# Performance work log

Hardware: AMD Instinct MI355X
Metric: run time of the kernel (lower is better)

## Reference

```python
import jax, jax.numpy as jnp
import numpy as np

TEMPERATURE = 0.05
BETA = 1.0
LAMBDA_THRESHOLD = 0.7


def setup_inputs() -> dict:
    key = jax.random.key(0)
    k1, k2 = jax.random.split(key)
    B, D = 8192, 256
    features = jax.random.normal(k1, (B, D), dtype=jnp.float32)
    labels = jax.random.randint(k2, (B,), 0, 100, dtype=jnp.int64)
    return {"features": features, "labels": labels}


def reference(features, labels):
    B = features.shape[0]
    eps = 1e-12
    # L2 normalize rows
    f = features / jnp.maximum(jnp.linalg.norm(features, axis=1, keepdims=True), eps)
    sim = jnp.matmul(f, f.T) / TEMPERATURE                      # [B, B]
    sim_max = jnp.max(sim, axis=1, keepdims=True)               # [B, 1]
    sim_stable = sim - sim_max

    same = (labels[:, None] == labels[None, :])
    eye = jnp.eye(B, dtype=bool)
    pos_mask = same & ~eye                                       # [B, B] bool

    # Denominator: logsumexp over all non-self entries per row
    exp_sim = jnp.exp(sim_stable) * (~eye)
    log_denom = jnp.log(jnp.sum(exp_sim, axis=1, keepdims=True) + eps) + sim_max  # [B,1]

    # SCL term: mean over positive pairs of (log_denom[i] - sim[i,j])
    pos_f = pos_mask.astype(sim.dtype)
    n_pos = jnp.sum(pos_f)
    scl_sum = jnp.sum(pos_f * (log_denom - sim))
    scl_loss = jnp.where(n_pos > 0, scl_sum / jnp.maximum(n_pos, 1.0), 0.0)

    # Relaxation term: per row, logsumexp over high-sim positive logits + baseline
    high = (sim * TEMPERATURE > LAMBDA_THRESHOLD) & pos_mask     # [B, B] bool
    neg_inf = jnp.asarray(-jnp.inf, sim.dtype)
    masked_logits = jnp.where(high, sim_stable, neg_inf)          # [B, B]
    baseline = (1.0 / TEMPERATURE) - sim_max                      # [B, 1]
    all_logits = jnp.concatenate([masked_logits, baseline], axis=1)  # [B, B+1]
    row_lse = jax.nn.logsumexp(all_logits, axis=1)                # [B]
    row_has = jnp.any(high, axis=1)
    n_high = jnp.sum(high.astype(sim.dtype))
    relax_sum = jnp.sum(jnp.where(row_has, row_lse, 0.0))
    relaxation_loss = jnp.where(n_high > 0, relax_sum / jnp.maximum(n_high, 1.0), 0.0)

    total = scl_loss + BETA * relaxation_loss
    return jnp.clip(total, 0.0, 10.0)
```

## Files before the change

kernel.cpp:

```cpp
#include <hip/hip_runtime.h>
#include <hip/hip_bf16.h>
#include <math.h>

#define B_N 8192
#define D_K 256
#define TILE 128
#define NT 1024
#define NBLK 64
#define NPAIR 2080
#define NCLS 100
#define KEXP 28.8539008177792681f
#define KCH 64
#define NCHUNK 4

typedef __attribute__((ext_vector_type(8))) short short8;
typedef __attribute__((ext_vector_type(4))) float f32x4;

template <bool V> struct BoolC { static constexpr bool value = V; };

__device__ __forceinline__ unsigned short f2bf(float x) {
    unsigned int u = __float_as_uint(x);
    unsigned int r = (u + 0x7FFFu + ((u >> 16) & 1u)) >> 16;
    return (unsigned short)r;
}

__device__ __forceinline__ void gload_lds16(const short* g, short* l) {
    __builtin_amdgcn_global_load_lds(
        (const __attribute__((address_space(1))) void*)g,
        (__attribute__((address_space(3))) void*)l, 16, 0, 0);
}

__device__ __forceinline__ float row_sum16(float v) {
    v += __int_as_float(__builtin_amdgcn_update_dpp(0, __float_as_int(v), 0xB1, 0xF, 0xF, true));
    v += __int_as_float(__builtin_amdgcn_update_dpp(0, __float_as_int(v), 0x4E, 0xF, 0xF, true));
    v += __int_as_float(__builtin_amdgcn_update_dpp(0, __float_as_int(v), 0x141, 0xF, 0xF, true));
    v += __int_as_float(__builtin_amdgcn_update_dpp(0, __float_as_int(v), 0x140, 0xF, 0xF, true));
    return v;
}

__global__ void prep_kernel(const float* __restrict__ feat, unsigned short* __restrict__ fnorm,
                            const int* __restrict__ labels, int* __restrict__ cnt,
                            float* __restrict__ gscal, double* __restrict__ accum,
                            unsigned int* __restrict__ done) {
    if (blockIdx.x == 0) {
        __shared__ int h[NCLS];
        int t = threadIdx.x;
        if (t < NCLS) h[t] = 0;
        if (t == 0) {
            gscal[0] = 0.f; gscal[1] = 0.f;
            accum[0] = 0.0; accum[1] = 0.0; accum[2] = 0.0;
            *done = 0u;
        }
        __syncthreads();
        for (int r = t; r < B_N; r += 256) atomicAdd(&h[labels[r]], 1);
        __syncthreads();
        if (t < NCLS) cnt[t] = h[t];
    }
    int wave = threadIdx.x >> 6, lane = threadIdx.x & 63;
    int row = blockIdx.x * 4 + wave;
    float4 v = *(const float4*)(feat + (size_t)row * D_K + lane * 4);
    float ss = v.x * v.x + v.y * v.y + v.z * v.z + v.w * v.w;
    #pragma unroll
    for (int off = 1; off < 64; off <<= 1) ss += __shfl_xor(ss, off);
    float inv = 1.0f / fmaxf(sqrtf(ss), 1e-12f);
    ushort4 o;
    o.x = f2bf(v.x * inv); o.y = f2bf(v.y * inv);
    o.z = f2bf(v.z * inv); o.w = f2bf(v.w * inv);
    *(ushort4*)(fnorm + (size_t)row * D_K + lane * 4) = o;
}

__global__ __launch_bounds__(NT, 8) void main_kernel(
        const unsigned short* __restrict__ fnorm, const int* __restrict__ labels,
        float2* __restrict__ G, float* __restrict__ gscal) {
    int bid = blockIdx.x;
    int b = (int)((sqrtf(8.0f * bid + 1.0f) - 1.0f) * 0.5f);
    while ((b + 1) * (b + 2) / 2 <= bid) ++b;
    while (b * (b + 1) / 2 > bid) --b;
    int a = bid - b * (b + 1) / 2;
    const int row0 = a * TILE, col0 = b * TILE;
    const bool diag = (a == b);

    __shared__ short As[2][TILE * KCH];
    __shared__ short Bs[2][TILE * KCH];
    __shared__ int Ls[2 * TILE];
    __shared__ int ghs[16];
    __shared__ float gps[16];

    const int tid = threadIdx.x;
    const int lane = tid & 63, wave = tid >> 6;
    const int wm = wave >> 2, wn = wave & 3;
    const int l15 = lane & 15, lhi = lane >> 4;
    const short* fn = (const short*)fnorm;

    const int rs = tid >> 3, cs = (tid & 7) ^ (rs & 7);
    const int uds = (tid & ~63) * 8;
    const int arow = (row0 + rs) * D_K + cs * 8;
    const int brow = (col0 + rs) * D_K + cs * 8;

    if (tid < 128) Ls[tid] = labels[row0 + tid];
    else if (tid < 256) Ls[tid] = labels[col0 + tid - 128];
    if (lane == 0) ghs[wave] = 0;

    gload_lds16(fn + arow, &As[0][uds]);
    if (!diag) gload_lds16(fn + brow, &Bs[0][uds]);

    f32x4 acc[2][2];
    #pragma unroll
    for (int i = 0; i < 2; i++)
        #pragma unroll
        for (int j = 0; j < 2; j++) acc[i][j] = {0.f, 0.f, 0.f, 0.f};

    #pragma unroll
    for (int kc = 0; kc < NCHUNK; ++kc) {
        const int cur = kc & 1;
        __syncthreads();
        if (kc < NCHUNK - 1) {
            const int nxt = cur ^ 1, ko = (kc + 1) * KCH;
            gload_lds16(fn + arow + ko, &As[nxt][uds]);
            if (!diag) gload_lds16(fn + brow + ko, &Bs[nxt][uds]);
        }
        const short* Asrc = As[cur];
        const short* Bsrc = diag ? As[cur] : Bs[cur];
        #pragma unroll
        for (int ks = 0; ks < 2; ++ks) {
            short8 af[2], bfr[2];
            const int ch8 = ((ks * 4 + lhi) ^ (l15 & 7)) * 8;
            #pragma unroll
            for (int mi = 0; mi < 2; mi++)
                af[mi] = *(const short8*)&Asrc[(wm * 32 + mi * 16 + l15) * KCH + ch8];
            #pragma unroll
            for (int ni = 0; ni < 2; ni++)
                bfr[ni] = *(const short8*)&Bsrc[(wn * 32 + ni * 16 + l15) * KCH + ch8];
            #pragma unroll
            for (int mi = 0; mi < 2; mi++)
                #pragma unroll
                for (int ni = 0; ni < 2; ni++)
                    acc[mi][ni] = __builtin_amdgcn_mfma_f32_16x16x32_bf16(af[mi], bfr[ni], acc[mi][ni], 0, 0, 0);
        }
    }
    __syncthreads();

    float2* Rbuf = (float2*)As[0];
    float2* Cbuf = (float2*)Bs[0];

    int lc[2], colg[2];
    #pragma unroll
    for (int ni = 0; ni < 2; ni++) {
        int c = wn * 32 + ni * 16 + l15;
        lc[ni] = Ls[128 + c];
        colg[ni] = col0 + c;
    }

    auto body = [&](auto DIAGC) {
        constexpr bool DIAG = decltype(DIAGC)::value;
        float cD[2] = {0.f, 0.f};
        float gp = 0.f;
        bool anyhi = false;

        #pragma unroll
        for (int mi = 0; mi < 2; mi++) {
            #pragma unroll
            for (int reg = 0; reg < 4; reg++) {
                int rloc = wm * 32 + mi * 16 + lhi * 4 + reg;
                int rowg = row0 + rloc;
                int lr = Ls[rloc];
                float d = 0.f;
                #pragma unroll
                for (int ni = 0; ni < 2; ni++) {
                    float dot = acc[mi][ni][reg];
                    float e = __builtin_exp2f((dot - 1.0f) * KEXP);
                    bool ns = !DIAG || (rowg != colg[ni]);
                    float ev = ns ? e : 0.f;
                    d += ev; cD[ni] += ev;
                    bool ps = ns && (lr == lc[ni]);
                    gp += ps ? dot : 0.f;
                    anyhi = anyhi | (ps & (dot > 0.7f));
                }
                d = row_sum16(d);
                if (l15 == 0) Rbuf[wn * 128 + rloc] = {d, 0.f};
            }
        }

        if (!DIAG) {
            #pragma unroll
            for (int ni = 0; ni < 2; ni++) {
                cD[ni] += __shfl_xor(cD[ni], 16);
                cD[ni] += __shfl_xor(cD[ni], 32);
            }
            if (lhi == 0) {
                #pragma unroll
                for (int ni = 0; ni < 2; ni++)
                    Cbuf[wm * 128 + wn * 32 + ni * 16 + l15] = {cD[ni], 0.f};
            }
        }

        gp = row_sum16(gp);
        gp += __shfl_xor(gp, 16);
        gp += __shfl_xor(gp, 32);
        if (lane == 0) gps[wave] = gp;

        if (__any(anyhi)) {
            float cR[2] = {0.f, 0.f};
            int nhi = 0;
            #pragma unroll
            for (int mi = 0; mi < 2; mi++) {
                #pragma unroll
                for (int reg = 0; reg < 4; reg++) {
                    int rloc = wm * 32 + mi * 16 + lhi * 4 + reg;
                    int rowg = row0 + rloc;
                    int lr = Ls[rloc];
                    float rx = 0.f;
                    #pragma unroll
                    for (int ni = 0; ni < 2; ni++) {
                        float dot = acc[mi][ni][reg];
                        bool ns = !DIAG || (rowg != colg[ni]);
                        bool hi = ns && (lr == lc[ni]) && (dot > 0.7f);
                        float e = hi ? __builtin_exp2f((dot - 1.0f) * KEXP) : 0.f;
                        rx += e; cR[ni] += e; nhi += hi ? 1 : 0;
                    }
                    rx = row_sum16(rx);
                    if (l15 == 0) Rbuf[wn * 128 + rloc].y = rx;
                }
            }
            if (!DIAG) {
                #pragma unroll
                for (int ni = 0; ni < 2; ni++) {
                    cR[ni] += __shfl_xor(cR[ni], 16);
                    cR[ni] += __shfl_xor(cR[ni], 32);
                }
                if (lhi == 0) {
                    #pragma unroll
                    for (int ni = 0; ni < 2; ni++)
                        Cbuf[wm * 128 + wn * 32 + ni * 16 + l15].y = cR[ni];
                }
            }
            #pragma unroll
            for (int off = 1; off < 64; off <<= 1) nhi += __shfl_xor(nhi, off);
            if (lane == 0) ghs[wave] = nhi;
        }
    };
    if (diag) body(BoolC<true>{});
    else body(BoolC<false>{});
    __syncthreads();

    if (tid < 128) {
        int r = tid;
        float2 a0 = Rbuf[r], a1 = Rbuf[128 + r], a2 = Rbuf[256 + r], a3 = Rbuf[384 + r];
        G[(size_t)b * B_N + row0 + r] = {a0.x + a1.x + a2.x + a3.x, a0.y + a1.y + a2.y + a3.y};
    } else if (tid < 256 && !diag) {
        int c = tid - 128;
        float2 a0 = Cbuf[c], a1 = Cbuf[128 + c], a2 = Cbuf[256 + c], a3 = Cbuf[384 + c];
        G[(size_t)a * B_N + col0 + c] = {a0.x + a1.x + a2.x + a3.x, a0.y + a1.y + a2.y + a3.y};
    }
    if (tid == 0) {
        float w = diag ? 1.0f : 2.0f;
        float gpt = 0.f;
        int tot = 0;
        #pragma unroll
        for (int i = 0; i < 16; i++) { gpt += gps[i]; tot += ghs[i]; }
        atomicAdd(&gscal[0], w * gpt);
        if (tot > 0) atomicAdd(&gscal[1], w * (float)tot);
    }
}

__global__ void finalize_kernel(const float2* __restrict__ G, const int* __restrict__ labels,
                                const int* __restrict__ cnt, const float* __restrict__ gscal,
                                double* __restrict__ accum, unsigned int* __restrict__ done,
                                float* __restrict__ out) {
    int lane = threadIdx.x & 63, q = threadIdx.x >> 6;
    int r = blockIdx.x * 64 + lane;
    float d = 0.f, rx = 0.f;
    #pragma unroll
    for (int s = 0; s < 16; ++s) {
        float2 g = G[(size_t)(q * 16 + s) * B_N + r];
        d += g.x; rx += g.y;
    }
    __shared__ float2 sh[4][64];
    sh[q][lane] = {d, rx};
    __syncthreads();
    if (threadIdx.x < 64) {
        int rr = blockIdx.x * 64 + threadIdx.x;
        float2 t0 = sh[0][threadIdx.x], t1 = sh[1][threadIdx.x];
        float2 t2 = sh[2][threadIdx.x], t3 = sh[3][threadIdx.x];
        float dd = t0.x + t1.x + t2.x + t3.x;
        float rr2 = t0.y + t1.y + t2.y + t3.y;
        float np = (float)(cnt[labels[rr]] - 1);
        float ld = logf(dd + 1e-12f) + 20.0f;
        double s1 = (double)np * (double)ld;
        double s2 = (double)np;
        double s3 = (rr2 > 0.f) ? (double)logf(rr2 + 1.0f) : 0.0;
        #pragma unroll
        for (int off = 1; off < 64; off <<= 1) {
            s1 += __shfl_xor(s1, off);
            s2 += __shfl_xor(s2, off);
            s3 += __shfl_xor(s3, off);
        }
        if (threadIdx.x == 0) {
            atomicAdd(&accum[0], s1);
            atomicAdd(&accum[1], s2);
            atomicAdd(&accum[2], s3);
            __threadfence();
            unsigned int tk = atomicAdd(done, 1u);
            if (tk == gridDim.x - 1) {
                double a1 = atomicAdd(&accum[0], 0.0);
                double a2 = atomicAdd(&accum[1], 0.0);
                double a3 = atomicAdd(&accum[2], 0.0);
                double gp = (double)gscal[0];
                double gh = (double)gscal[1];
                double scl = (a2 > 0.0) ? (a1 - 20.0 * gp) / fmax(a2, 1.0) : 0.0;
                double rel = (gh > 0.0) ? a3 / fmax(gh, 1.0) : 0.0;
                double tot = scl + rel;
                tot = fmin(fmax(tot, 0.0), 10.0);
                out[0] = (float)tot;
            }
        }
    }
}

extern "C" void kernel_launch(void* const* d_in, const int* in_sizes, int n_in,
                              void* d_out, int out_size, void* d_ws, size_t ws_size,
                              hipStream_t stream) {
    const float* feat = (const float*)d_in[0];
    const int* labels = (const int*)d_in[1];
    float* out = (float*)d_out;
    char* ws = (char*)d_ws;

    unsigned short* fnorm = (unsigned short*)(ws);
    float2* G          = (float2*)(ws + (size_t)4 * 1024 * 1024);
    int*    cnt        = (int*)(ws + (size_t)8 * 1024 * 1024);
    float*  gscal      = (float*)(ws + (size_t)8 * 1024 * 1024 + 1024);
    double* accum      = (double*)(ws + (size_t)8 * 1024 * 1024 + 2048);
    unsigned int* done = (unsigned int*)(ws + (size_t)8 * 1024 * 1024 + 3072);

    prep_kernel<<<B_N / 4, 256, 0, stream>>>(feat, fnorm, labels, cnt, gscal, accum, done);
    main_kernel<<<NPAIR, NT, 0, stream>>>(fnorm, labels, G, gscal);
    finalize_kernel<<<B_N / 64, 256, 0, stream>>>(G, labels, cnt, gscal, accum, done, out);
    (void)in_sizes; (void)n_in; (void)out_size; (void)ws_size;
}
```

Baseline: 122.2 us.

## Make main kernel persistent with atomic tile queue and prefetch next tile

Replaces the one-block-per-tile-pair grid with a persistent grid of 512 blocks that pull tile indices from a global atomic counter. The first K-chunk of the next tile is prefetched into LDS while the current tile's epilogue runs, and LDS fragment offsets are hoisted out of the loop. The prep kernel is also enlarged to 1024 threads per block and initializes the work counter. The intent is to hide block launch and prologue latency. In exchange it adds an atomic per tile and serializes each block's tiles, which may leave the load less evenly balanced at the tail.

```diff
diff --git a/kernel.cpp b/kernel.cpp
--- a/kernel.cpp
+++ b/kernel.cpp
@@ -12,6 +12,7 @@
 #define KEXP 28.8539008177792681f
 #define KCH 64
 #define NCHUNK 4
+#define GRID_MAIN 512
 
 typedef __attribute__((ext_vector_type(8))) short short8;
 typedef __attribute__((ext_vector_type(4))) float f32x4;
@@ -38,10 +39,19 @@
     return v;
 }
 
-__global__ void prep_kernel(const float* __restrict__ feat, unsigned short* __restrict__ fnorm,
-                            const int* __restrict__ labels, int* __restrict__ cnt,
-                            float* __restrict__ gscal, double* __restrict__ accum,
-                            unsigned int* __restrict__ done) {
+__device__ __forceinline__ void decode_pair(int t, int& a, int& b) {
+    int bb = (int)((sqrtf(8.0f * t + 1.0f) - 1.0f) * 0.5f);
+    while ((bb + 1) * (bb + 2) / 2 <= t) ++bb;
+    while (bb * (bb + 1) / 2 > t) --bb;
+    a = t - bb * (bb + 1) / 2;
+    b = bb;
+}
+
+__global__ __launch_bounds__(1024) void prep_kernel(
+        const float* __restrict__ feat, unsigned short* __restrict__ fnorm,
+        const int* __restrict__ labels, int* __restrict__ cnt,
+        float* __restrict__ gscal, double* __restrict__ accum,
+        unsigned int* __restrict__ done, unsigned int* __restrict__ wctr) {
     if (blockIdx.x == 0) {
         __shared__ int h[NCLS];
         int t = threadIdx.x;
@@ -50,14 +60,15 @@
             gscal[0] = 0.f; gscal[1] = 0.f;
             accum[0] = 0.0; accum[1] = 0.0; accum[2] = 0.0;
             *done = 0u;
+            *wctr = GRID_MAIN;
         }
         __syncthreads();
-        for (int r = t; r < B_N; r += 256) atomicAdd(&h[labels[r]], 1);
+        for (int r = t; r < B_N; r += 1024) atomicAdd(&h[labels[r]], 1);
         __syncthreads();
         if (t < NCLS) cnt[t] = h[t];
     }
     int wave = threadIdx.x >> 6, lane = threadIdx.x & 63;
-    int row = blockIdx.x * 4 + wave;
+    int row = blockIdx.x * 16 + wave;
     float4 v = *(const float4*)(feat + (size_t)row * D_K + lane * 4);
     float ss = v.x * v.x + v.y * v.y + v.z * v.z + v.w * v.w;
     #pragma unroll
@@ -71,20 +82,13 @@
 
 __global__ __launch_bounds__(NT, 8) void main_kernel(
         const unsigned short* __restrict__ fnorm, const int* __restrict__ labels,
-        float2* __restrict__ G, float* __restrict__ gscal) {
-    int bid = blockIdx.x;
-    int b = (int)((sqrtf(8.0f * bid + 1.0f) - 1.0f) * 0.5f);
-    while ((b + 1) * (b + 2) / 2 <= bid) ++b;
-    while (b * (b + 1) / 2 > bid) --b;
-    int a = bid - b * (b + 1) / 2;
-    const int row0 = a * TILE, col0 = b * TILE;
-    const bool diag = (a == b);
-
+        float2* __restrict__ G, float* __restrict__ gscal, unsigned int* __restrict__ wctr) {
     __shared__ short As[2][TILE * KCH];
     __shared__ short Bs[2][TILE * KCH];
     __shared__ int Ls[2 * TILE];
     __shared__ int ghs[16];
     __shared__ float gps[16];
+    __shared__ int nxs;
 
     const int tid = threadIdx.x;
     const int lane = tid & 63, wave = tid >> 6;
@@ -94,114 +98,98 @@
 
     const int rs = tid >> 3, cs = (tid & 7) ^ (rs & 7);
     const int uds = (tid & ~63) * 8;
-    const int arow = (row0 + rs) * D_K + cs * 8;
-    const int brow = (col0 + rs) * D_K + cs * 8;
+    const int stg = rs * D_K + cs * 8;
+
+    const int ch8_0 = (lhi ^ (l15 & 7)) * 8;
+    const int ch8_1 = ((4 + lhi) ^ (l15 & 7)) * 8;
+    int aof[2][2], bof[2][2];
+    #pragma unroll
+    for (int mi = 0; mi < 2; mi++) {
+        aof[0][mi] = (wm * 32 + mi * 16 + l15) * KCH + ch8_0;
+        aof[1][mi] = (wm * 32 + mi * 16 + l15) * KCH + ch8_1;
+        bof[0][mi] = (wn * 32 + mi * 16 + l15) * KCH + ch8_0;
+        bof[1][mi] = (wn * 32 + mi * 16 + l15) * KCH + ch8_1;
+    }
+
+    int tile = blockIdx.x, a, b;
+    decode_pair(tile, a, b);
+    int row0 = a * TILE, col0 = b * TILE;
+    bool diag = (a == b);
 
     if (tid < 128) Ls[tid] = labels[row0 + tid];
     else if (tid < 256) Ls[tid] = labels[col0 + tid - 128];
-    if (lane == 0) ghs[wave] = 0;
-
-    gload_lds16(fn + arow, &As[0][uds]);
-    if (!diag) gload_lds16(fn + brow, &Bs[0][uds]);
-
-    f32x4 acc[2][2];
-    #pragma unroll
-    for (int i = 0; i < 2; i++)
+
+    gload_lds16(fn + row0 * D_K + stg, &As[1][uds]);
+    if (!diag) gload_lds16(fn + col0 * D_K + stg, &Bs[1][uds]);
+
+    for (;;) {
+        const int arow = row0 * D_K + stg;
+        const int brow = col0 * D_K + stg;
+
+        f32x4 acc[2][2];
         #pragma unroll
-        for (int j = 0; j < 2; j++) acc[i][j] = {0.f, 0.f, 0.f, 0.f};
-
-    #pragma unroll
-    for (int kc = 0; kc < NCHUNK; ++kc) {
-        const int cur = kc & 1;
+        for (int i = 0; i < 2; i++)
+            #pragma unroll
+            for (int j = 0; j < 2; j++) acc[i][j] = {0.f, 0.f, 0.f, 0.f};
+
+        #pragma unroll
+        for (int kc = 0; kc < NCHUNK; ++kc) {
+            const int buf = (kc + 1) & 1;
+            __syncthreads();
+            if (kc == 0) {
+                if (tid == 0) nxs = atomicAdd(wctr, 1u);
+                if (lane == 0) ghs[wave] = 0;
+            }
+            if (kc < NCHUNK - 1) {
+                const int nb = buf ^ 1, ko = (kc + 1) * KCH;
+                gload_lds16(fn + arow + ko, &As[nb][uds]);
+                if (!diag) gload_lds16(fn + brow + ko, &Bs[nb][uds]);
+            }
+            const short* Asrc = As[buf];
+            const short* Bsrc = diag ? As[buf] : Bs[buf];
+            #pragma unroll
+            for (int ks = 0; ks < 2; ++ks) {
+                short8 af[2], bfr[2];
+                #pragma unroll
+                for (int mi = 0; mi < 2; mi++) af[mi] = *(const short8*)&Asrc[aof[ks][mi]];
+                #pragma unroll
+                for (int ni = 0; ni < 2; ni++) bfr[ni] = *(const short8*)&Bsrc[bof[ks][ni]];
+                #pragma unroll
+                for (int mi = 0; mi < 2; mi++)
+                    #pragma unroll
+                    for (int ni = 0; ni < 2; ni++)
+                        acc[mi][ni] = __builtin_amdgcn_mfma_f32_16x16x32_bf16(af[mi], bfr[ni], acc[mi][ni], 0, 0, 0);
+            }
+        }
         __syncthreads();
-        if (kc < NCHUNK - 1) {
-            const int nxt = cur ^ 1, ko = (kc + 1) * KCH;
-            gload_lds16(fn + arow + ko, &As[nxt][uds]);
-            if (!diag) gload_lds16(fn + brow + ko, &Bs[nxt][uds]);
-        }
-        const short* Asrc = As[cur];
-        const short* Bsrc = diag ? As[cur] : Bs[cur];
+
+        const int nx = nxs;
+        int na = 0, nb2 = 0, nrow0 = 0, ncol0 = 0;
+        bool ndiag = false;
+        if (nx < NPAIR) {
+            decode_pair(nx, na, nb2);
+            nrow0 = na * TILE; ncol0 = nb2 * TILE; ndiag = (na == nb2);
+            gload_lds16(fn + nrow0 * D_K + stg, &As[1][uds]);
+            if (!ndiag) gload_lds16(fn + ncol0 * D_K + stg, &Bs[1][uds]);
+        }
+
+        float2* Rbuf = (float2*)As[0];
+        float2* Cbuf = (float2*)Bs[0];
+
+        int lc[2], colg[2];
         #pragma unroll
-        for (int ks = 0; ks < 2; ++ks) {
-            short8 af[2], bfr[2];
-            const int ch8 = ((ks * 4 + lhi) ^ (l15 & 7)) * 8;
-            #pragma unroll
-            for (int mi = 0; mi < 2; mi++)
-                af[mi] = *(const short8*)&Asrc[(wm * 32 + mi * 16 + l15) * KCH + ch8];
-            #pragma unroll
-            for (int ni = 0; ni < 2; ni++)
-                bfr[ni] = *(const short8*)&Bsrc[(wn * 32 + ni * 16 + l15) * KCH + ch8];
-            #pragma unroll
-            for (int mi = 0; mi < 2; mi++)
-                #pragma unroll
-                for (int ni = 0; ni < 2; ni++)
-                    acc[mi][ni] = __builtin_amdgcn_mfma_f32_16x16x32_bf16(af[mi], bfr[ni], acc[mi][ni], 0, 0, 0);
-        }
-    }
-    __syncthreads();
-
-    float2* Rbuf = (float2*)As[0];
-    float2* Cbuf = (float2*)Bs[0];
-
-    int lc[2], colg[2];
-    #pragma unroll
-    for (int ni = 0; ni < 2; ni++) {
-        int c = wn * 32 + ni * 16 + l15;
-        lc[ni] = Ls[128 + c];
-        colg[ni] = col0 + c;
-    }
-
-    auto body = [&](auto DIAGC) {
-        constexpr bool DIAG = decltype(DIAGC)::value;
-        float cD[2] = {0.f, 0.f};
-        float gp = 0.f;
-        bool anyhi = false;
-
-        #pragma unroll
-        for (int mi = 0; mi < 2; mi++) {
-            #pragma unroll
-            for (int reg = 0; reg < 4; reg++) {
-                int rloc = wm * 32 + mi * 16 + lhi * 4 + reg;
-                int rowg = row0 + rloc;
-                int lr = Ls[rloc];
-                float d = 0.f;
-                #pragma unroll
-                for (int ni = 0; ni < 2; ni++) {
-                    float dot = acc[mi][ni][reg];
-                    float e = __builtin_exp2f((dot - 1.0f) * KEXP);
-                    bool ns = !DIAG || (rowg != colg[ni]);
-                    float ev = ns ? e : 0.f;
-                    d += ev; cD[ni] += ev;
-                    bool ps = ns && (lr == lc[ni]);
-                    gp += ps ? dot : 0.f;
-                    anyhi = anyhi | (ps & (dot > 0.7f));
-                }
-                d = row_sum16(d);
-                if (l15 == 0) Rbuf[wn * 128 + rloc] = {d, 0.f};
-            }
-        }
-
-        if (!DIAG) {
-            #pragma unroll
-            for (int ni = 0; ni < 2; ni++) {
-                cD[ni] += __shfl_xor(cD[ni], 16);
-                cD[ni] += __shfl_xor(cD[ni], 32);
-            }
-            if (lhi == 0) {
-                #pragma unroll
-                for (int ni = 0; ni < 2; ni++)
-                    Cbuf[wm * 128 + wn * 32 + ni * 16 + l15] = {cD[ni], 0.f};
-            }
-        }
-
-        gp = row_sum16(gp);
-        gp += __shfl_xor(gp, 16);
-        gp += __shfl_xor(gp, 32);
-        if (lane == 0) gps[wave] = gp;
-
-        if (__any(anyhi)) {
-            float cR[2] = {0.f, 0.f};
-            int nhi = 0;
+        for (int ni = 0; ni < 2; ni++) {
+            int c = wn * 32 + ni * 16 + l15;
+            lc[ni] = Ls[128 + c];
+            colg[ni] = col0 + c;
+        }
+
+        auto body = [&](auto DIAGC) {
+            constexpr bool DIAG = decltype(DIAGC)::value;
+            float cD[2] = {0.f, 0.f};
+            float gp = 0.f;
+            bool anyhi = false;
+
             #pragma unroll
             for (int mi = 0; mi < 2; mi++) {
                 #pragma unroll
@@ -209,57 +197,108 @@
                     int rloc = wm * 32 + mi * 16 + lhi * 4 + reg;
                     int rowg = row0 + rloc;
                     int lr = Ls[rloc];
-                    float rx = 0.f;
+                    float d = 0.f;
                     #pragma unroll
                     for (int ni = 0; ni < 2; ni++) {
                         float dot = acc[mi][ni][reg];
+                        float e = __builtin_exp2f((dot - 1.0f) * KEXP);
                         bool ns = !DIAG || (rowg != colg[ni]);
-                        bool hi = ns && (lr == lc[ni]) && (dot > 0.7f);
-                        float e = hi ? __builtin_exp2f((dot - 1.0f) * KEXP) : 0.f;
-                        rx += e; cR[ni] += e; nhi += hi ? 1 : 0;
+                        float ev = ns ? e : 0.f;
+                        d += ev; cD[ni] += ev;
+                        bool ps = ns && (lr == lc[ni]);
+                        gp += ps ? dot : 0.f;
+                        anyhi = anyhi | (ps & (dot > 0.7f));
                     }
-                    rx = row_sum16(rx);
-                    if (l15 == 0) Rbuf[wn * 128 + rloc].y = rx;
-                }
-            }
+                    d = row_sum16(d);
+                    if (l15 == 0) Rbuf[wn * 128 + rloc] = {d, 0.f};
+                }
+            }
+
             if (!DIAG) {
                 #pragma unroll
                 for (int ni = 0; ni < 2; ni++) {
-                    cR[ni] += __shfl_xor(cR[ni], 16);
-                    cR[ni] += __shfl_xor(cR[ni], 32);
+                    cD[ni] += __shfl_xor(cD[ni], 16);
+                    cD[ni] += __shfl_xor(cD[ni], 32);
                 }
                 if (lhi == 0) {
                     #pragma unroll
                     for (int ni = 0; ni < 2; ni++)
-                        Cbuf[wm * 128 + wn * 32 + ni * 16 + l15].y = cR[ni];
-                }
-            }
+                        Cbuf[wm * 128 + wn * 32 + ni * 16 + l15] = {cD[ni], 0.f};
+                }
+            }
+
+            gp = row_sum16(gp);
+            gp += __shfl_xor(gp, 16);
+            gp += __shfl_xor(gp, 32);
+            if (lane == 0) gps[wave] = gp;
+
+            if (__any(anyhi)) {
+                float cR[2] = {0.f, 0.f};
+                int nhi = 0;
+                #pragma unroll
+                for (int mi = 0; mi < 2; mi++) {
+                    #pragma unroll
+                    for (int reg = 0; reg < 4; reg++) {
+                        int rloc = wm * 32 + mi * 16 + lhi * 4 + reg;
+                        int rowg = row0 + rloc;
+                        int lr = Ls[rloc];
+                        float rx = 0.f;
+                        #pragma unroll
+                        for (int ni = 0; ni < 2; ni++) {
+                            float dot = acc[mi][ni][reg];
+                            bool ns = !DIAG || (rowg != colg[ni]);
+                            bool hi = ns && (lr == lc[ni]) && (dot > 0.7f);
+                            float e = hi ? __builtin_exp2f((dot - 1.0f) * KEXP) : 0.f;
+                            rx += e; cR[ni] += e; nhi += hi ? 1 : 0;
+                        }
+                        rx = row_sum16(rx);
+                        if (l15 == 0) Rbuf[wn * 128 + rloc].y = rx;
+                    }
+                }
+                if (!DIAG) {
+                    #pragma unroll
+                    for (int ni = 0; ni < 2; ni++) {
+                        cR[ni] += __shfl_xor(cR[ni], 16);
+                        cR[ni] += __shfl_xor(cR[ni], 32);
+                    }
+                    if (lhi == 0) {
+                        #pragma unroll
+                        for (int ni = 0; ni < 2; ni++)
+                            Cbuf[wm * 128 + wn * 32 + ni * 16 + l15].y = cR[ni];
+                    }
+                }
+                #pragma unroll
+                for (int off = 1; off < 64; off <<= 1) nhi += __shfl_xor(nhi, off);
+                if (lane == 0) ghs[wave] = nhi;
+            }
+        };
+        if (diag) body(BoolC<true>{});
+        else body(BoolC<false>{});
+        __syncthreads();
+
+        if (tid < 128) {
+            int r = tid;
+            float2 a0 = Rbuf[r], a1 = Rbuf[128 + r], a2 = Rbuf[256 + r], a3 = Rbuf[384 + r];
+            G[(size_t)b * B_N + row0 + r] = {a0.x + a1.x + a2.x + a3.x, a0.y + a1.y + a2.y + a3.y};
+        } else if (tid < 256 && !diag) {
+            int c = tid - 128;
+            float2 a0 = Cbuf[c], a1 = Cbuf[128 + c], a2 = Cbuf[256 + c], a3 = Cbuf[384 + c];
+            G[(size_t)a * B_N + col0 + c] = {a0.x + a1.x + a2.x + a3.x, a0.y + a1.y + a2.y + a3.y};
+        }
+        if (tid == 0) {
+            float w = diag ? 1.0f : 2.0f;
+            float gpt = 0.f;
+            int tot = 0;
             #pragma unroll
-            for (int off = 1; off < 64; off <<= 1) nhi += __shfl_xor(nhi, off);
-            if (lane == 0) ghs[wave] = nhi;
-        }
-    };
-    if (diag) body(BoolC<true>{});
-    else body(BoolC<false>{});
-    __syncthreads();
-
-    if (tid < 128) {
-        int r = tid;
-        float2 a0 = Rbuf[r], a1 = Rbuf[128 + r], a2 = Rbuf[256 + r], a3 = Rbuf[384 + r];
-        G[(size_t)b * B_N + row0 + r] = {a0.x + a1.x + a2.x + a3.x, a0.y + a1.y + a2.y + a3.y};
-    } else if (tid < 256 && !diag) {
-        int c = tid - 128;
-        float2 a0 = Cbuf[c], a1 = Cbuf[128 + c], a2 = Cbuf[256 + c], a3 = Cbuf[384 + c];
-        G[(size_t)a * B_N + col0 + c] = {a0.x + a1.x + a2.x + a3.x, a0.y + a1.y + a2.y + a3.y};
-    }
-    if (tid == 0) {
-        float w = diag ? 1.0f : 2.0f;
-        float gpt = 0.f;
-        int tot = 0;
-        #pragma unroll
-        for (int i = 0; i < 16; i++) { gpt += gps[i]; tot += ghs[i]; }
-        atomicAdd(&gscal[0], w * gpt);
-        if (tot > 0) atomicAdd(&gscal[1], w * (float)tot);
+            for (int i = 0; i < 16; i++) { gpt += gps[i]; tot += ghs[i]; }
+            atomicAdd(&gscal[0], w * gpt);
+            if (tot > 0) atomicAdd(&gscal[1], w * (float)tot);
+        }
+
+        if (nx >= NPAIR) break;
+        if (tid < 128) Ls[tid] = labels[nrow0 + tid];
+        else if (tid < 256) Ls[tid] = labels[ncol0 + tid - 128];
+        a = na; b = nb2; row0 = nrow0; col0 = ncol0; diag = ndiag;
     }
 }
 
@@ -331,9 +370,10 @@
     float*  gscal      = (float*)(ws + (size_t)8 * 1024 * 1024 + 1024);
     double* accum      = (double*)(ws + (size_t)8 * 1024 * 1024 + 2048);
     unsigned int* done = (unsigned int*)(ws + (size_t)8 * 1024 * 1024 + 3072);
-
-    prep_kernel<<<B_N / 4, 256, 0, stream>>>(feat, fnorm, labels, cnt, gscal, accum, done);
-    main_kernel<<<NPAIR, NT, 0, stream>>>(fnorm, labels, G, gscal);
+    unsigned int* wctr = (unsigned int*)(ws + (size_t)8 * 1024 * 1024 + 3136);
+
+    prep_kernel<<<B_N / 16, 1024, 0, stream>>>(feat, fnorm, labels, cnt, gscal, accum, done, wctr);
+    main_kernel<<<GRID_MAIN, NT, 0, stream>>>(fnorm, labels, G, gscal, wctr);
     finalize_kernel<<<B_N / 64, 256, 0, stream>>>(G, labels, cnt, gscal, accum, done, out);
     (void)in_sizes; (void)n_in; (void)out_size; (void)ws_size;
 }
```

Measured after the change: 138.9 us. 13.6% more time.
